# Performance work log

Measured on AMD Instinct MI355X. Metric: run time of the kernel, lower is better.

## Reference

```python
import jax, jax.numpy as jnp
import numpy as np

LOG2PI = float(np.log(2.0 * np.pi))


def setup_inputs() -> dict:
    key = jax.random.key(0)
    ks = jax.random.split(key, 5)
    B, T, XD, C = 128, 2050, 6, 64
    return {
        "x": jax.random.normal(ks[0], (B, T, XD), jnp.float32),
        "observation_means": jax.random.uniform(ks[1], (C, XD), dtype=jnp.float32),
        "observation_stddevs": jax.random.uniform(ks[2], (C, XD), dtype=jnp.float32),
        "log_A": jax.random.normal(ks[3], (C, C), jnp.float32),
        "log_pi": jax.random.normal(ks[4], (C,), jnp.float32),
    }


def _emission_logprob(x, means, stds):
    # Normal(means[:, :4], relu(stds[:, :4]) + 0.1).log_prob(x[:, :, :4]) summed over feat dim
    mu = means[:, :4]                       # (C,4)
    sigma = jax.nn.relu(stds[:, :4]) + 0.1  # (C,4)
    z = (x[:, :, None, :4] - mu) / sigma    # (B,T,C,4)
    return jnp.sum(-0.5 * z * z - jnp.log(sigma) - 0.5 * LOG2PI, axis=-1)  # (B,T,C)


def _forward_scalers(logp, log_A, log_pi):
    # scaled HMM forward pass; returns per-step log normalizers (T,B)
    a0 = logp[:, 0] + log_pi
    s0 = jax.nn.logsumexp(a0, axis=-1)
    a0n = a0 - s0[:, None]

    def step(a_prev, lp_t):
        a = lp_t + jax.nn.logsumexp(a_prev[:, :, None] + log_A[None], axis=1)
        s = jax.nn.logsumexp(a, axis=-1)
        return a - s[:, None], s

    _, s_rest = jax.lax.scan(step, a0n, jnp.swapaxes(logp[:, 1:], 0, 1))
    return jnp.concatenate([s0[None], s_rest], axis=0)  # (T,B)


def _viterbi(logp, log_A, log_pi):
    d0 = logp[:, 0] + log_pi  # (B,C)

    def step(d_prev, lp_t):
        scores = d_prev[:, :, None] + log_A[None]  # (B,C_prev,C_cur)
        psi_t = jnp.argmax(scores, axis=1)
        d = jnp.max(scores, axis=1) + lp_t
        return d, psi_t

    d_last, psi = jax.lax.scan(step, d0, jnp.swapaxes(logp[:, 1:], 0, 1))  # psi: (T-1,B,C)
    c_last = jnp.argmax(d_last, axis=-1)  # (B,)

    def back(c_next, psi_t):
        c_t = jnp.take_along_axis(psi_t, c_next[:, None], axis=1)[:, 0]
        return c_t, c_t

    _, cs = jax.lax.scan(back, c_last, psi, reverse=True)  # (T-1,B)
    c = jnp.concatenate([cs, c_last[None]], axis=0)  # (T,B)
    return jnp.swapaxes(c, 0, 1)  # (B,T)


def reference(x, observation_means, observation_stddevs, log_A, log_pi):
    logA = jax.nn.log_softmax(log_A, axis=1)
    logpi = jax.nn.log_softmax(log_pi, axis=0)
    logp = _emission_logprob(x, observation_means, observation_stddevs)  # (B,T,C)
    scalers = _forward_scalers(logp, logA, logpi)                         # (T,B)
    logp_x = jnp.sum(scalers, axis=0)                                     # (B,)
    c_est = _viterbi(logp, logA, logpi)                                   # (B,T) int
    return logp_x, c_est
```

## Files before the change

kernel.cpp:

```cpp
#include <hip/hip_runtime.h>

#define T_LEN 2050
#define B_SZ 128
#define NCHUNK 33
#define NEMIS 65600
#define HL2PI 0.91893853320467274178f

__device__ __forceinline__ float waveMax(float v) {
#pragma unroll
    for (int off = 32; off >= 1; off >>= 1)
        v = fmaxf(v, __shfl_xor(v, off, 64));
    return v;
}
__device__ __forceinline__ float waveSum(float v) {
#pragma unroll
    for (int off = 32; off >= 1; off >>= 1)
        v += __shfl_xor(v, off, 64);
    return v;
}
__device__ __forceinline__ void waveArgmax(float& v, int& idx) {
#pragma unroll
    for (int off = 32; off >= 1; off >>= 1) {
        float ov = __shfl_xor(v, off, 64);
        int   oi = __shfl_xor(idx, off, 64);
        if (ov > v || (ov == v && oi < idx)) { v = ov; idx = oi; }
    }
}
__device__ __forceinline__ void cfence() { asm volatile("" ::: "memory"); }

__device__ __forceinline__ float dppSumAll(float v) {
#define SSTEP(ctrl) { int t_ = __builtin_amdgcn_update_dpp(0, __float_as_int(v), ctrl, 0xf, 0xf, true); \
                      v = v + __int_as_float(t_); }
    SSTEP(0x111) SSTEP(0x112) SSTEP(0x114) SSTEP(0x118) SSTEP(0x142) SSTEP(0x143)
#undef SSTEP
    return __int_as_float(__builtin_amdgcn_readlane(__float_as_int(v), 63));
}
__device__ __forceinline__ float dppMaxAll(float v) {
#define MSTEP(ctrl) { int t_ = __builtin_amdgcn_update_dpp(__float_as_int(v), __float_as_int(v), ctrl, 0xf, 0xf, false); \
                      v = fmaxf(v, __int_as_float(t_)); }
    MSTEP(0x111) MSTEP(0x112) MSTEP(0x114) MSTEP(0x118) MSTEP(0x142) MSTEP(0x143)
#undef MSTEP
    return __int_as_float(__builtin_amdgcn_readlane(__float_as_int(v), 63));
}

extern "C" __global__ __launch_bounds__(256)
void hmm_emis(const float* __restrict__ x,
              const float* __restrict__ means,
              const float* __restrict__ stds,
              const float* __restrict__ logA_in,
              const float* __restrict__ logpi_in,
              float* __restrict__ buf,
              float* __restrict__ m_pre,
              float* __restrict__ lAg,
              float* __restrict__ lpig)
{
    __shared__ float la[64 * 65];
    __shared__ float rowlse[64];

    if (blockIdx.x == NEMIS) {
        if (threadIdx.x >= 64) return;
        const int j = threadIdx.x;
#pragma unroll
        for (int k = 0; k < 64; ++k)
            la[k * 65 + j] = logA_in[k * 64 + j];
        cfence();
        {
            float m = -1e30f;
#pragma unroll
            for (int k = 0; k < 64; ++k) m = fmaxf(m, la[j * 65 + k]);
            float s = 0.f;
#pragma unroll
            for (int k = 0; k < 64; ++k) s += expf(la[j * 65 + k] - m);
            rowlse[j] = m + logf(s);
        }
        cfence();
        {
            float v = logpi_in[j];
            float m = waveMax(v);
            float s = waveSum(expf(v - m));
            lpig[j] = v - (m + logf(s));
        }
        float4* o = (float4*)lAg;
#pragma unroll
        for (int k = 0; k < 16; ++k) {
            float4 v;
            v.x = la[(4 * k + 0) * 65 + j] - rowlse[4 * k + 0];
            v.y = la[(4 * k + 1) * 65 + j] - rowlse[4 * k + 1];
            v.z = la[(4 * k + 2) * 65 + j] - rowlse[4 * k + 2];
            v.w = la[(4 * k + 3) * 65 + j] - rowlse[4 * k + 3];
            o[j * 16 + k] = v;
        }
        return;
    }

    const int wid = blockIdx.x * 4 + (threadIdx.x >> 6);
    const int j = threadIdx.x & 63;
    const int t = wid >> 7;
    const int b = wid & 127;

    const float* xt = x + ((size_t)b * T_LEN + t) * 6;
    float x0 = xt[0], x1 = xt[1], x2 = xt[2], x3 = xt[3];

    float mu0 = means[j * 6 + 0], mu1 = means[j * 6 + 1];
    float mu2 = means[j * 6 + 2], mu3 = means[j * 6 + 3];
    float sg0 = fmaxf(stds[j * 6 + 0], 0.f) + 0.1f;
    float sg1 = fmaxf(stds[j * 6 + 1], 0.f) + 0.1f;
    float sg2 = fmaxf(stds[j * 6 + 2], 0.f) + 0.1f;
    float sg3 = fmaxf(stds[j * 6 + 3], 0.f) + 0.1f;
    float ls0 = logf(sg0), ls1 = logf(sg1), ls2 = logf(sg2), ls3 = logf(sg3);

    float z0 = (x0 - mu0) / sg0, z1 = (x1 - mu1) / sg1;
    float z2 = (x2 - mu2) / sg2, z3 = (x3 - mu3) / sg3;
    float e0 = ((-0.5f * z0) * z0 - ls0) - HL2PI;
    float e1 = ((-0.5f * z1) * z1 - ls1) - HL2PI;
    float e2 = ((-0.5f * z2) * z2 - ls2) - HL2PI;
    float e3 = ((-0.5f * z3) * z3 - ls3) - HL2PI;
    float lp = ((e0 + e1) + e2) + e3;

    buf[((size_t)b * T_LEN + t) * 64 + j] = lp;
    float mm = waveMax(lp);
    if (j == 0) m_pre[(size_t)b * T_LEN + t] = mm;
}

extern "C" __global__ __launch_bounds__(64, 1)
void hmm_main(const float* __restrict__ x,
              const float* __restrict__ means,
              const float* __restrict__ stds,
              const float* __restrict__ lAg,
              const float* __restrict__ lpig,
              float* __restrict__ out,
              float* __restrict__ buf,
              const float* __restrict__ m_pre,
              int* __restrict__ c_last)
{
    __shared__ __align__(16) float xs[12304];
    __shared__ __align__(16) float pbuf[64];

    const int j   = threadIdx.x;
    const int bid = blockIdx.x;
    const bool is_fwd = (bid < B_SZ);
    const int b = is_fwd ? bid : bid - B_SZ;

    float lpi = lpig[j];
    const float4* pv = (const float4*)pbuf;

    if (is_fwd) {
        {
            const float4* xg4 = (const float4*)(x + (size_t)b * T_LEN * 6);
            float4* xs4 = (float4*)xs;
            for (int i = j; i < 3075; i += 64) xs4[i] = xg4[i];
        }
        float mu0 = means[j * 6 + 0], mu1 = means[j * 6 + 1];
        float mu2 = means[j * 6 + 2], mu3 = means[j * 6 + 3];
        float sg0 = fmaxf(stds[j * 6 + 0], 0.f) + 0.1f;
        float sg1 = fmaxf(stds[j * 6 + 1], 0.f) + 0.1f;
        float sg2 = fmaxf(stds[j * 6 + 2], 0.f) + 0.1f;
        float sg3 = fmaxf(stds[j * 6 + 3], 0.f) + 0.1f;
        float ls0 = logf(sg0), ls1 = logf(sg1), ls2 = logf(sg2), ls3 = logf(sg3);
        float i0 = 1.f / sg0, i1 = 1.f / sg1, i2 = 1.f / sg2, i3 = 1.f / sg3;
        float cst = -(ls0 + ls1 + ls2 + ls3) - 4.f * HL2PI;

        float Ac[64];
        {
            const float4* g = (const float4*)lAg;
#pragma unroll
            for (int k = 0; k < 16; ++k) {
                float4 v = g[j * 16 + k];
                Ac[4 * k + 0] = __expf(v.x); Ac[4 * k + 1] = __expf(v.y);
                Ac[4 * k + 2] = __expf(v.z); Ac[4 * k + 3] = __expf(v.w);
            }
        }
        cfence();

        float z0 = (xs[0] - mu0) * i0, z1 = (xs[1] - mu1) * i1;
        float z2 = (xs[2] - mu2) * i2, z3 = (xs[3] - mu3) * i3;
        float a0 = (cst - 0.5f * (z0 * z0 + z1 * z1 + z2 * z2 + z3 * z3)) + lpi;
        float m0a = dppMaxAll(a0);
        float u = __expf(a0 - m0a);
        float s0 = dppSumAll(u);
        double acc = (double)(m0a + __logf(s0));
        u *= (1.0f / s0);
        pbuf[j] = u;
        float4 rr[16];
#pragma unroll
        for (int k = 0; k < 16; ++k) rr[k] = pv[k];

        const float* mp = m_pre + (size_t)b * T_LEN;
        float g0 = mp[1], g1 = mp[2], g2 = mp[3], g3 = mp[4];

#pragma unroll 1
        for (int t = 1; t < T_LEN; ++t) {
            float mm_c = g0; g0 = g1; g1 = g2; g2 = g3;
            int tp = t + 4; if (tp > T_LEN - 1) tp = T_LEN - 1;
            g3 = mp[tp];

            int o = t * 6;
            float y0 = xs[o], y1 = xs[o + 1], y2 = xs[o + 2], y3 = xs[o + 3];
            float w0 = (y0 - mu0) * i0, w1 = (y1 - mu1) * i1;
            float w2 = (y2 - mu2) * i2, w3 = (y3 - mu3) * i3;
            float lp = cst - 0.5f * (w0 * w0 + w1 * w1 + w2 * w2 + w3 * w3);
            float e_c = __expf(lp - mm_c);

            float q0 = 0.f, q1 = 0.f, q2 = 0.f, q3 = 0.f;
#pragma unroll
            for (int k = 0; k < 16; ++k) {
                float4 pp = rr[k];
                q0 = fmaf(pp.x, Ac[4 * k + 0], q0);
                q1 = fmaf(pp.y, Ac[4 * k + 1], q1);
                q2 = fmaf(pp.z, Ac[4 * k + 2], q2);
                q3 = fmaf(pp.w, Ac[4 * k + 3], q3);
            }
            u = ((q0 + q1) + (q2 + q3)) * e_c;
            acc += (double)mm_c;
            if ((t & 3) == 0) {
                float ss = dppSumAll(u);
                acc += (double)__logf(ss);
                u *= (1.0f / ss);
            }

            pbuf[j] = u;
#pragma unroll
            for (int k = 0; k < 16; ++k) rr[k] = pv[k];
        }
        float sf = dppSumAll(u);
        acc += (double)__logf(sf);
        if (j == 0) out[b] = (float)acc;
    } else {
        float lA[64];
        {
            const float4* g = (const float4*)lAg;
#pragma unroll
            for (int k = 0; k < 16; ++k) {
                float4 v = g[j * 16 + k];
                lA[4 * k + 0] = v.x; lA[4 * k + 1] = v.y;
                lA[4 * k + 2] = v.z; lA[4 * k + 3] = v.w;
            }
        }
        float* bb = buf + (size_t)b * T_LEN * 64 + j;

        float dn = bb[0] + lpi;
        float l0 = bb[64], l1 = bb[128], l2 = bb[192], l3 = bb[256];
        bb[0] = dn;
        pbuf[j] = dn;
        float4 rr[16];
#pragma unroll
        for (int k = 0; k < 16; ++k) rr[k] = pv[k];

#pragma unroll 1
        for (int t = 1; t < T_LEN; ++t) {
            float lp_c = l0; l0 = l1; l1 = l2; l2 = l3;
            int tp = t + 4; if (tp > T_LEN - 1) tp = T_LEN - 1;
            l3 = bb[(size_t)tp * 64];

            float m0 = -3.4e38f, m1 = -3.4e38f, m2 = -3.4e38f, m3 = -3.4e38f;
#pragma unroll
            for (int k = 0; k < 16; ++k) {
                float4 dd = rr[k];
                m0 = fmaxf(m0, dd.x + lA[4 * k + 0]);
                m1 = fmaxf(m1, dd.y + lA[4 * k + 1]);
                m2 = fmaxf(m2, dd.z + lA[4 * k + 2]);
                m3 = fmaxf(m3, dd.w + lA[4 * k + 3]);
            }
            dn = fmaxf(fmaxf(m0, m1), fmaxf(m2, m3)) + lp_c;

            bb[(size_t)t * 64] = dn;
            pbuf[j] = dn;
#pragma unroll
            for (int k = 0; k < 16; ++k) rr[k] = pv[k];
        }

        float vv = dn; int idx = j;
        waveArgmax(vv, idx);
        if (j == 0) c_last[b] = idx;
    }
}

extern "C" __global__ __launch_bounds__(256)
void hmm_psi(const float* __restrict__ buf,
             const float* __restrict__ lAg,
             unsigned char* __restrict__ psi)
{
    __shared__ __align__(16) float sd[4][64];
    const int warp = threadIdx.x >> 6;
    const int j = threadIdx.x & 63;
    const int wid = blockIdx.x * 4 + warp;

    float lA[64];
    {
        const float4* g = (const float4*)lAg;
#pragma unroll
        for (int k = 0; k < 16; ++k) {
            float4 v = g[j * 16 + k];
            lA[4 * k + 0] = v.x; lA[4 * k + 1] = v.y;
            lA[4 * k + 2] = v.z; lA[4 * k + 3] = v.w;
        }
    }
    const float4* dv = (const float4*)sd[warp];
    const int NP = 2049 * B_SZ;
    const int p0 = wid * 32;
    const int p1 = (p0 + 32 < NP) ? p0 + 32 : NP;

#pragma unroll 2
    for (int p = p0; p < p1; ++p) {
        const int b = p / 2049;
        const int t = p - b * 2049 + 1;
        float dval = buf[((size_t)b * T_LEN + (t - 1)) * 64 + j];
        sd[warp][j] = dval;

        float bv0 = -3.4e38f, bv1 = -3.4e38f, bv2 = -3.4e38f, bv3 = -3.4e38f;
        int bi0 = 0, bi1 = 1, bi2 = 2, bi3 = 3;
#pragma unroll
        for (int k = 0; k < 16; ++k) {
            float4 dd = dv[k];
            float v0 = dd.x + lA[4 * k + 0];
            float v1 = dd.y + lA[4 * k + 1];
            float v2 = dd.z + lA[4 * k + 2];
            float v3 = dd.w + lA[4 * k + 3];
            if (v0 > bv0) { bv0 = v0; bi0 = 4 * k + 0; }
            if (v1 > bv1) { bv1 = v1; bi1 = 4 * k + 1; }
            if (v2 > bv2) { bv2 = v2; bi2 = 4 * k + 2; }
            if (v3 > bv3) { bv3 = v3; bi3 = 4 * k + 3; }
        }
        float best = bv0; int bidx = bi0;
        if (bv1 > best || (bv1 == best && bi1 < bidx)) { best = bv1; bidx = bi1; }
        if (bv2 > best || (bv2 == best && bi2 < bidx)) { best = bv2; bidx = bi2; }
        if (bv3 > best || (bv3 == best && bi3 < bidx)) { best = bv3; bidx = bi3; }

        psi[((size_t)t * B_SZ + b) * 64 + j] = (unsigned char)bidx;
    }
}

extern "C" __global__ __launch_bounds__(256)
void hmm_compose(const unsigned char* __restrict__ psi,
                 unsigned char* __restrict__ mt)
{
    const int w = blockIdx.x * 4 + (threadIdx.x >> 6);
    const int j = threadIdx.x & 63;
    const int g = w % NCHUNK;
    const int b = w / NCHUNK;
    const int e = (g < NCHUNK - 1) ? g * 64 + 64 : (T_LEN - 1);
    int M = j;
    for (int t = e; t >= g * 64 + 1; --t)
        M = psi[((size_t)t * B_SZ + b) * 64 + M];
    mt[((size_t)g * B_SZ + b) * 64 + j] = (unsigned char)M;
}

extern "C" __global__ __launch_bounds__(64, 1)
void hmm_fill(const unsigned char* __restrict__ psi,
              const unsigned char* __restrict__ mt,
              const int* __restrict__ c_last,
              float* __restrict__ out)
{
    __shared__ int sb[NCHUNK];
    const int b = blockIdx.x;
    const int g = threadIdx.x;
    const int cl = c_last[b];
    if (g == 0) {
        int cur = cl;
        for (int q = NCHUNK - 1; q >= 0; --q) {
            cur = mt[((size_t)q * B_SZ + b) * 64 + cur];
            sb[q] = cur;
        }
    }
    cfence();
    float* oc = out + B_SZ + (size_t)b * T_LEN;
    if (g == NCHUNK) {
        oc[T_LEN - 1] = (float)cl;
    } else if (g < NCHUNK) {
        const int e = (g < NCHUNK - 1) ? g * 64 + 64 : (T_LEN - 1);
        int s = (g < NCHUNK - 1) ? sb[g + 1] : cl;
        for (int t = e; t >= g * 64 + 1; --t) {
            s = psi[((size_t)t * B_SZ + b) * 64 + s];
            oc[t - 1] = (float)s;
        }
    }
}

extern "C" void kernel_launch(void* const* d_in, const int* in_sizes, int n_in,
                              void* d_out, int out_size, void* d_ws, size_t ws_size,
                              hipStream_t stream)
{
    const float* x      = (const float*)d_in[0];
    const float* means  = (const float*)d_in[1];
    const float* stds   = (const float*)d_in[2];
    const float* logA   = (const float*)d_in[3];
    const float* logpi  = (const float*)d_in[4];
    float* out = (float*)d_out;

    char* base = (char*)d_ws;
    float*         buf   = (float*)base;
    unsigned char* psi   = (unsigned char*)(base + 67174400);
    float*         m_pre = (float*)(base + 67174400);
    unsigned char* mt    = (unsigned char*)(base + 83968000);
    int*           cl    = (int*)(base + 84238336);
    float*         lAg   = (float*)(base + 84238848);
    float*         lpig  = (float*)(base + 84255232);

    hipLaunchKernelGGL(hmm_emis, dim3(NEMIS + 1), dim3(256), 0, stream,
                       x, means, stds, logA, logpi, buf, m_pre, lAg, lpig);
    hipLaunchKernelGGL(hmm_main, dim3(2 * B_SZ), dim3(64), 0, stream,
                       x, means, stds, lAg, lpig, out, buf, m_pre, cl);
    hipLaunchKernelGGL(hmm_psi, dim3(2050), dim3(256), 0, stream, buf, lAg, psi);
    hipLaunchKernelGGL(hmm_compose, dim3((NCHUNK * B_SZ) / 4), dim3(256), 0, stream, psi, mt);
    hipLaunchKernelGGL(hmm_fill, dim3(B_SZ), dim3(64), 0, stream, psi, mt, cl, out);
}
```

Before: 1.070 ms.

## Replace LDS state broadcast with DPP wave-rotate in HMM recurrences

Both the forward and Viterbi recurrences stop writing the 64-state vector to shared memory and reading it back as 16 float4 loads every step. Each lane now walks its own state value around the wavefront with wave_ror:1 DPP moves. To match, the transition matrix is pre-rotated per lane through an LDS staging buffer. This removes the per-step LDS write/read round trip, but it puts a serial chain of 63 dependent DPP moves on the critical path of every timestep.

Result: slower. 1.502 ms (+40.4%).

```diff
diff --git a/kernel.cpp b/kernel.cpp
--- a/kernel.cpp
+++ b/kernel.cpp
@@ -41,6 +41,11 @@
     MSTEP(0x111) MSTEP(0x112) MSTEP(0x114) MSTEP(0x118) MSTEP(0x142) MSTEP(0x143)
 #undef MSTEP
     return __int_as_float(__builtin_amdgcn_readlane(__float_as_int(v), 63));
+}
+__device__ __forceinline__ float ror1(float v) {
+    int r = __builtin_amdgcn_update_dpp(__float_as_int(v), __float_as_int(v),
+                                        0x13C, 0xf, 0xf, false);
+    return __int_as_float(r);
 }
 
 extern "C" __global__ __launch_bounds__(256)
@@ -134,7 +139,7 @@
               int* __restrict__ c_last)
 {
     __shared__ __align__(16) float xs[12304];
-    __shared__ __align__(16) float pbuf[64];
+    __shared__ __align__(16) float cbuf[4096];
 
     const int j   = threadIdx.x;
     const int bid = blockIdx.x;
@@ -142,7 +147,18 @@
     const int b = is_fwd ? bid : bid - B_SZ;
 
     float lpi = lpig[j];
-    const float4* pv = (const float4*)pbuf;
+
+    float lAr[64];
+    {
+        const float4* g = (const float4*)lAg;
+        float4* cb4 = (float4*)(cbuf + j * 64);
+#pragma unroll
+        for (int k = 0; k < 16; ++k) cb4[k] = g[j * 16 + k];
+        cfence();
+#pragma unroll
+        for (int s = 0; s < 64; ++s)
+            lAr[s] = cbuf[j * 64 + ((j + s) & 63)];
+    }
 
     if (is_fwd) {
         {
@@ -160,16 +176,9 @@
         float i0 = 1.f / sg0, i1 = 1.f / sg1, i2 = 1.f / sg2, i3 = 1.f / sg3;
         float cst = -(ls0 + ls1 + ls2 + ls3) - 4.f * HL2PI;
 
-        float Ac[64];
-        {
-            const float4* g = (const float4*)lAg;
-#pragma unroll
-            for (int k = 0; k < 16; ++k) {
-                float4 v = g[j * 16 + k];
-                Ac[4 * k + 0] = __expf(v.x); Ac[4 * k + 1] = __expf(v.y);
-                Ac[4 * k + 2] = __expf(v.z); Ac[4 * k + 3] = __expf(v.w);
-            }
-        }
+        float Acr[64];
+#pragma unroll
+        for (int s = 0; s < 64; ++s) Acr[s] = __expf(lAr[s]);
         cfence();
 
         float z0 = (xs[0] - mu0) * i0, z1 = (xs[1] - mu1) * i1;
@@ -180,10 +189,6 @@
         float s0 = dppSumAll(u);
         double acc = (double)(m0a + __logf(s0));
         u *= (1.0f / s0);
-        pbuf[j] = u;
-        float4 rr[16];
-#pragma unroll
-        for (int k = 0; k < 16; ++k) rr[k] = pv[k];
 
         const float* mp = m_pre + (size_t)b * T_LEN;
         float g0 = mp[1], g1 = mp[2], g2 = mp[3], g3 = mp[4];
@@ -201,14 +206,15 @@
             float lp = cst - 0.5f * (w0 * w0 + w1 * w1 + w2 * w2 + w3 * w3);
             float e_c = __expf(lp - mm_c);
 
+            float r = u;
             float q0 = 0.f, q1 = 0.f, q2 = 0.f, q3 = 0.f;
 #pragma unroll
-            for (int k = 0; k < 16; ++k) {
-                float4 pp = rr[k];
-                q0 = fmaf(pp.x, Ac[4 * k + 0], q0);
-                q1 = fmaf(pp.y, Ac[4 * k + 1], q1);
-                q2 = fmaf(pp.z, Ac[4 * k + 2], q2);
-                q3 = fmaf(pp.w, Ac[4 * k + 3], q3);
+            for (int s = 0; s < 64; s += 4) {
+                q0 = fmaf(r, Acr[s + 0], q0); r = ror1(r);
+                q1 = fmaf(r, Acr[s + 1], q1); r = ror1(r);
+                q2 = fmaf(r, Acr[s + 2], q2); r = ror1(r);
+                q3 = fmaf(r, Acr[s + 3], q3);
+                if (s + 4 < 64) r = ror1(r);
             }
             u = ((q0 + q1) + (q2 + q3)) * e_c;
             acc += (double)mm_c;
@@ -217,34 +223,16 @@
                 acc += (double)__logf(ss);
                 u *= (1.0f / ss);
             }
-
-            pbuf[j] = u;
-#pragma unroll
-            for (int k = 0; k < 16; ++k) rr[k] = pv[k];
         }
         float sf = dppSumAll(u);
         acc += (double)__logf(sf);
         if (j == 0) out[b] = (float)acc;
     } else {
-        float lA[64];
-        {
-            const float4* g = (const float4*)lAg;
-#pragma unroll
-            for (int k = 0; k < 16; ++k) {
-                float4 v = g[j * 16 + k];
-                lA[4 * k + 0] = v.x; lA[4 * k + 1] = v.y;
-                lA[4 * k + 2] = v.z; lA[4 * k + 3] = v.w;
-            }
-        }
         float* bb = buf + (size_t)b * T_LEN * 64 + j;
 
         float dn = bb[0] + lpi;
         float l0 = bb[64], l1 = bb[128], l2 = bb[192], l3 = bb[256];
         bb[0] = dn;
-        pbuf[j] = dn;
-        float4 rr[16];
-#pragma unroll
-        for (int k = 0; k < 16; ++k) rr[k] = pv[k];
 
 #pragma unroll 1
         for (int t = 1; t < T_LEN; ++t) {
@@ -252,21 +240,19 @@
             int tp = t + 4; if (tp > T_LEN - 1) tp = T_LEN - 1;
             l3 = bb[(size_t)tp * 64];
 
+            float r = dn;
             float m0 = -3.4e38f, m1 = -3.4e38f, m2 = -3.4e38f, m3 = -3.4e38f;
 #pragma unroll
-            for (int k = 0; k < 16; ++k) {
-                float4 dd = rr[k];
-                m0 = fmaxf(m0, dd.x + lA[4 * k + 0]);
-                m1 = fmaxf(m1, dd.y + lA[4 * k + 1]);
-                m2 = fmaxf(m2, dd.z + lA[4 * k + 2]);
-                m3 = fmaxf(m3, dd.w + lA[4 * k + 3]);
+            for (int s = 0; s < 64; s += 4) {
+                m0 = fmaxf(m0, r + lAr[s + 0]); r = ror1(r);
+                m1 = fmaxf(m1, r + lAr[s + 1]); r = ror1(r);
+                m2 = fmaxf(m2, r + lAr[s + 2]); r = ror1(r);
+                m3 = fmaxf(m3, r + lAr[s + 3]);
+                if (s + 4 < 64) r = ror1(r);
             }
             dn = fmaxf(fmaxf(m0, m1), fmaxf(m2, m3)) + lp_c;
 
             bb[(size_t)t * 64] = dn;
-            pbuf[j] = dn;
-#pragma unroll
-            for (int k = 0; k < 16; ++k) rr[k] = pv[k];
         }
 
         float vv = dn; int idx = j;
```
